# Kernel tuning notes

Hardware: AMD Instinct MI355X
Metric: run time of the kernel (lower is better)

The kernel has to match this reference:

```python
import jax, jax.numpy as jnp
import numpy as np

N, E, B = 50000, 400000, 16
H, D = 4, 64  # heads, per-head out feats
NUM_LAYERS = 4
NEG_SLOPE = 0.2


def setup_inputs() -> dict:
    key = jax.random.key(0)
    ks = jax.random.split(key, 12)
    inp = {
        "feat": jax.random.normal(ks[0], (N, 16), jnp.float32),
        "is_root": jax.random.uniform(ks[1], (N,), jnp.float32),
        "src": jax.random.randint(ks[2], (E,), 0, N, jnp.int32),
        "dst": jax.random.randint(ks[3], (E,), 0, N, jnp.int32),
        "graph_id": jnp.sort(jax.random.randint(ks[4], (N,), 0, B, jnp.int32)),
        "W_in": jax.random.normal(ks[5], (16, 64), jnp.float32) / jnp.sqrt(16.0),
        "b_in": jnp.zeros((64,), jnp.float32),
        "W_src": jax.random.normal(ks[6], (128, 256), jnp.float32) / jnp.sqrt(128.0),
        "b_src": jnp.zeros((256,), jnp.float32),
        "W_dst": jax.random.normal(ks[7], (128, 256), jnp.float32) / jnp.sqrt(128.0),
        "b_dst": jnp.zeros((256,), jnp.float32),
        "attn": jax.random.normal(ks[8], (H, D), jnp.float32) / jnp.sqrt(float(D)),
        "W_out": jax.random.normal(ks[9], (64, 32), jnp.float32) / jnp.sqrt(64.0),
        "b_out": jnp.zeros((32,), jnp.float32),
    }
    return inp


def _gatv2_layer(x, W_src, b_src, W_dst, b_dst, attn, src, dst, n_nodes):
    # DGL GATv2Conv: e_ij = a . LeakyReLU(W_src x_j + W_dst x_i); softmax over in-edges of i.
    fs = (x @ W_src + b_src).reshape(n_nodes, H, D)
    fd = (x @ W_dst + b_dst).reshape(n_nodes, H, D)
    e = jax.nn.leaky_relu(fs[src] + fd[dst], NEG_SLOPE)          # [E,H,D]
    logits = jnp.einsum("ehd,hd->eh", e, attn)                    # [E,H]
    m = jax.ops.segment_max(logits, dst, num_segments=n_nodes)    # [N,H]
    ex = jnp.exp(logits - m[dst])
    denom = jax.ops.segment_sum(ex, dst, num_segments=n_nodes)    # [N,H]
    alpha = ex / denom[dst]                                       # [E,H]
    msg = fs[src] * alpha[:, :, None]                             # [E,H,D]
    rst = jax.ops.segment_sum(msg, dst, num_segments=n_nodes)     # [N,H,D]
    return jnp.tanh(rst)


def reference(feat, is_root, src, dst, graph_id,
              W_in, b_in, W_src, b_src, W_dst, b_dst, attn, W_out, b_out):
    n_nodes = feat.shape[0]
    h0 = feat @ W_in + b_in                                       # [N,64]
    h = h0
    for _ in range(NUM_LAYERS):
        x = jnp.concatenate([h, h0], axis=1)                      # [N,128]
        h = _gatv2_layer(x, W_src, b_src, W_dst, b_dst, attn, src, dst, n_nodes).sum(axis=1)  # [N,64]
    hg = jax.ops.segment_sum(h * is_root[:, None], graph_id, num_segments=B)  # [B,64]
    return hg @ W_out + b_out                                     # [B,32]
```

## Files before the change

### kernel.cpp

```cpp
#include <hip/hip_runtime.h>
#include <math.h>

#define N_NODES 50000
#define N_EDGES 400000
#define N_GRAPHS 16
#define HEADS 4
#define NEG_SLOPE 0.2f
#define MAX_DEG 64

typedef __attribute__((ext_vector_type(8))) short short8;
typedef __attribute__((ext_vector_type(4))) float floatx4;
typedef _Float16 half_t;
typedef _Float16 half2_t __attribute__((ext_vector_type(2)));
typedef _Float16 half4_t __attribute__((ext_vector_type(4)));

__device__ __forceinline__ unsigned short f2bf(float x) {
    union { float f; unsigned int u; } v; v.f = x;
    unsigned int r = v.u + 0x7fffu + ((v.u >> 16) & 1u);
    return (unsigned short)(r >> 16);
}
__device__ __forceinline__ float bf2f(unsigned short b) {
    union { unsigned int u; float f; } v; v.u = ((unsigned int)b) << 16;
    return v.f;
}
__device__ __forceinline__ half2_t u2h2(unsigned int u) {
    union { unsigned int i; half2_t h; } v; v.i = u;
    return v.h;
}
__device__ __forceinline__ float fast_tanh(float x) {
    float e = __expf(2.f * x);
    return 1.f - 2.f / (e + 1.f);
}
__device__ __forceinline__ half2_t lrelu2(half2_t e) {
    half2_t s = e * (half2_t){(half_t)NEG_SLOPE, (half_t)NEG_SLOPE};
    return __builtin_elementwise_max(e, s);
}
__device__ __forceinline__ float dot2acc(half2_t a, half2_t b, float c) {
#if __has_builtin(__builtin_amdgcn_fdot2)
    return __builtin_amdgcn_fdot2(a, b, c, false);
#else
    return c + (float)a[0] * (float)b[0] + (float)a[1] * (float)b[1];
#endif
}

__global__ __launch_bounds__(256) void k_h0_pack(const float* __restrict__ feat,
                                                 const float* __restrict__ W_in,
                                                 const float* __restrict__ b_in,
                                                 unsigned short* __restrict__ h0,
                                                 const float* __restrict__ Wsrc,
                                                 const float* __restrict__ Wdst,
                                                 unsigned short* __restrict__ Wpack,
                                                 int* __restrict__ cursor,
                                                 float* __restrict__ hg) {
    int bid = blockIdx.x;
    if (bid < 12500) {
        int idx = bid * 256 + threadIdx.x;
        int node = idx >> 6, d = idx & 63;
        float acc = b_in[d];
        #pragma unroll
        for (int k = 0; k < 16; k++) acc += feat[node * 16 + k] * W_in[k * 64 + d];
        h0[idx] = f2bf(acc);
    } else if (bid < 12756) {
        int pb = bid - 12500;
        int mat = pb >> 7;
        int idx = (pb & 127) * 256 + threadIdx.x;
        const float* W = mat ? Wdst : Wsrc;
        int j = idx & 7;
        int lane = (idx >> 3) & 63;
        int q = (idx >> 9) & 3;
        int t = (idx >> 11) & 15;
        int col = t * 16 + (lane & 15);
        int k = q * 32 + (lane >> 4) * 8 + j;
        Wpack[mat * 32768 + idx] = f2bf(W[k * 256 + col]);
    } else if (bid < 12952) {
        int idx = (bid - 12756) * 256 + threadIdx.x;
        if (idx < N_NODES) cursor[idx] = 0;
    } else {
        for (int i = threadIdx.x; i < N_GRAPHS * 64; i += 256) hg[i] = 0.f;
    }
}

__global__ __launch_bounds__(256) void k_fill(const int* __restrict__ src, const int* __restrict__ dst,
                                              int* __restrict__ cursor, int* __restrict__ csr_pad, int e) {
    int i = blockIdx.x * 256 + threadIdx.x;
    if (i >= e) return;
    int d = dst[i];
    int slot = atomicAdd(&cursor[d], 1);
    if (slot < MAX_DEG) csr_pad[d * MAX_DEG + slot] = src[i];
}

__global__ __launch_bounds__(256) void k_gemm(const unsigned short* __restrict__ h,
                                              const unsigned short* __restrict__ h0,
                                              const unsigned short* __restrict__ Wpack,
                                              const float* __restrict__ bsrc,
                                              const float* __restrict__ bdst,
                                              half_t* __restrict__ fs,
                                              half_t* __restrict__ fd, int n) {
    __shared__ half_t tile[32][264];
    int mat = blockIdx.y;
    const unsigned short* Wp = Wpack + mat * 32768;
    const float* bias = mat ? bdst : bsrc;
    half_t* out = mat ? fd : fs;
    int wave = threadIdx.x >> 6, lane = threadIdx.x & 63;
    int quad = lane >> 4, m16 = lane & 15;
    int fhalf = wave & 1;
    int ngrp = wave >> 1;
    int node0 = blockIdx.x * 32 + ngrp * 16;

    floatx4 acc[8];
    #pragma unroll
    for (int t = 0; t < 8; t++) acc[t] = (floatx4){0.f, 0.f, 0.f, 0.f};

    int r = node0 + m16;
    if (r > n - 1) r = n - 1;

    #pragma unroll
    for (int q = 0; q < 4; q++) {
        int kk = q * 32 + quad * 8;
        const unsigned short* base = (kk < 64) ? (h + (size_t)r * 64 + kk)
                                               : (h0 + (size_t)r * 64 + (kk - 64));
        short8 x = *(const short8*)base;
        #pragma unroll
        for (int t = 0; t < 8; t++) {
            int tt = fhalf * 8 + t;
            short8 w = *(const short8*)(Wp + ((size_t)(tt * 4 + q) * 64 + lane) * 8);
            acc[t] = __builtin_amdgcn_mfma_f32_16x16x32_bf16(w, x, acc[t], 0, 0, 0);
        }
    }
    int lrow = ngrp * 16 + m16;
    #pragma unroll
    for (int t = 0; t < 8; t++) {
        int fbase = (fhalf * 8 + t) * 16 + quad * 4;
        float4 bb = *(const float4*)(bias + fbase);
        half4_t ov = { (half_t)(acc[t][0] + bb.x), (half_t)(acc[t][1] + bb.y),
                       (half_t)(acc[t][2] + bb.z), (half_t)(acc[t][3] + bb.w) };
        *(half4_t*)&tile[lrow][fbase] = ov;
    }
    __syncthreads();
    int base = blockIdx.x * 32;
    for (int i = threadIdx.x; i < 1024; i += 256) {
        int row = i >> 5, seg = i & 31;
        int node = base + row;
        if (node < n) {
            uint4 v = *(const uint4*)&tile[row][seg * 8];
            *(uint4*)(out + (size_t)node * 256 + seg * 8) = v;
        }
    }
}

__global__ __launch_bounds__(256) void k_agg(const half_t* __restrict__ fs,
                                             const half_t* __restrict__ fd,
                                             const int* __restrict__ cnt,
                                             const int* __restrict__ csr_pad,
                                             const float* __restrict__ attn,
                                             unsigned short* __restrict__ hout, int n) {
    int wave = threadIdx.x >> 6;
    int lane = threadIdx.x & 63;
    int node = blockIdx.x * 4 + wave;
    if (node >= n) return;
    int slot = lane >> 5;
    int foff = ((lane >> 3) & 3) * 64 + (lane & 7) * 8;
    unsigned boff = (unsigned)foff * 2;
    const char* fsb = (const char*)fs;

    half2_t at2[4];
    {
        float4 a0 = *(const float4*)(attn + foff);
        float4 a1 = *(const float4*)(attn + foff + 4);
        at2[0] = (half2_t){(half_t)a0.x, (half_t)a0.y};
        at2[1] = (half2_t){(half_t)a0.z, (half_t)a0.w};
        at2[2] = (half2_t){(half_t)a1.x, (half_t)a1.y};
        at2[3] = (half2_t){(half_t)a1.z, (half_t)a1.w};
    }
    half2_t fd2[4];
    {
        uint4 u = *(const uint4*)(fd + (size_t)node * 256 + foff);
        fd2[0] = u2h2(u.x); fd2[1] = u2h2(u.y); fd2[2] = u2h2(u.z); fd2[3] = u2h2(u.w);
    }

    int deg = cnt[node];
    if (deg > MAX_DEG) deg = MAX_DEG;
    int eid = 0;
    if (lane < deg) eid = csr_pad[node * MAX_DEG + lane];

    float l = 0.f;
    half2_t zero2 = {(half_t)0.f, (half_t)0.f};
    half2_t acc2[4] = {zero2, zero2, zero2, zero2};

    for (int j = 0; j < deg; j += 8) {
        int last = deg - 1;
        int i0 = j + slot, i1 = j + 2 + slot, i2 = j + 4 + slot, i3 = j + 6 + slot;
        bool v0 = i0 < deg, v1 = i1 < deg, v2 = i2 < deg, v3 = i3 < deg;
        int s0 = __shfl(eid, v0 ? i0 : last, 64);
        int s1 = __shfl(eid, v1 ? i1 : last, 64);
        int s2 = __shfl(eid, v2 ? i2 : last, 64);
        int s3 = __shfl(eid, v3 ? i3 : last, 64);
        uint4 g0 = *(const uint4*)(fsb + (((unsigned)s0 << 9) + boff));
        uint4 g1 = *(const uint4*)(fsb + (((unsigned)s1 << 9) + boff));
        uint4 g2 = *(const uint4*)(fsb + (((unsigned)s2 << 9) + boff));
        uint4 g3 = *(const uint4*)(fsb + (((unsigned)s3 << 9) + boff));
        half2_t f0[4] = {u2h2(g0.x), u2h2(g0.y), u2h2(g0.z), u2h2(g0.w)};
        half2_t f1[4] = {u2h2(g1.x), u2h2(g1.y), u2h2(g1.z), u2h2(g1.w)};
        half2_t f2[4] = {u2h2(g2.x), u2h2(g2.y), u2h2(g2.z), u2h2(g2.w)};
        half2_t f3[4] = {u2h2(g3.x), u2h2(g3.y), u2h2(g3.z), u2h2(g3.w)};
        float p0 = 0.f, p1 = 0.f, p2 = 0.f, p3 = 0.f;
        #pragma unroll
        for (int k = 0; k < 4; k++) {
            p0 = dot2acc(at2[k], lrelu2(f0[k] + fd2[k]), p0);
            p1 = dot2acc(at2[k], lrelu2(f1[k] + fd2[k]), p1);
            p2 = dot2acc(at2[k], lrelu2(f2[k] + fd2[k]), p2);
            p3 = dot2acc(at2[k], lrelu2(f3[k] + fd2[k]), p3);
        }
        p0 += __shfl_xor(p0, 1, 64); p1 += __shfl_xor(p1, 1, 64);
        p2 += __shfl_xor(p2, 1, 64); p3 += __shfl_xor(p3, 1, 64);
        p0 += __shfl_xor(p0, 2, 64); p1 += __shfl_xor(p1, 2, 64);
        p2 += __shfl_xor(p2, 2, 64); p3 += __shfl_xor(p3, 2, 64);
        p0 += __shfl_xor(p0, 4, 64); p1 += __shfl_xor(p1, 4, 64);
        p2 += __shfl_xor(p2, 4, 64); p3 += __shfl_xor(p3, 4, 64);
        float w0 = v0 ? __expf(fminf(p0, 80.f)) : 0.f;
        float w1 = v1 ? __expf(fminf(p1, 80.f)) : 0.f;
        float w2 = v2 ? __expf(fminf(p2, 80.f)) : 0.f;
        float w3 = v3 ? __expf(fminf(p3, 80.f)) : 0.f;
        l += (w0 + w1) + (w2 + w3);
        half_t hw0 = (half_t)w0, hw1 = (half_t)w1, hw2 = (half_t)w2, hw3 = (half_t)w3;
        half2_t w02 = {hw0, hw0}, w12 = {hw1, hw1}, w22 = {hw2, hw2}, w32 = {hw3, hw3};
        #pragma unroll
        for (int k = 0; k < 4; k++) {
            acc2[k] += w02 * f0[k];
            acc2[k] += w12 * f1[k];
            acc2[k] += w22 * f2[k];
            acc2[k] += w32 * f3[k];
        }
    }
    l += __shfl_xor(l, 32, 64);
    #pragma unroll
    for (int k = 0; k < 4; k++) {
        float t = __builtin_bit_cast(float, acc2[k]);
        t = __shfl_xor(t, 32, 64);
        acc2[k] += __builtin_bit_cast(half2_t, t);
    }

    float inv = (l > 0.f) ? 1.f / l : 0.f;
    half2_t a0 = slot ? acc2[2] : acc2[0];
    half2_t a1 = slot ? acc2[3] : acc2[1];
    float o0 = fast_tanh((float)a0[0] * inv);
    float o1 = fast_tanh((float)a0[1] * inv);
    float o2 = fast_tanh((float)a1[0] * inv);
    float o3 = fast_tanh((float)a1[1] * inv);
    o0 += __shfl_xor(o0, 8, 64);  o0 += __shfl_xor(o0, 16, 64);
    o1 += __shfl_xor(o1, 8, 64);  o1 += __shfl_xor(o1, 16, 64);
    o2 += __shfl_xor(o2, 8, 64);  o2 += __shfl_xor(o2, 16, 64);
    o3 += __shfl_xor(o3, 8, 64);  o3 += __shfl_xor(o3, 16, 64);
    if ((lane & 31) < 8) {
        ushort4 ov = {f2bf(o0), f2bf(o1), f2bf(o2), f2bf(o3)};
        *(ushort4*)(hout + (size_t)node * 64 + (lane & 7) * 8 + slot * 4) = ov;
    }
}

__global__ __launch_bounds__(256) void k_readout(const unsigned short* __restrict__ h,
                                                 const float* __restrict__ is_root,
                                                 const int* __restrict__ gid, float* __restrict__ hg, int n) {
    int wave = threadIdx.x >> 6, lane = threadIdx.x & 63;
    int start = blockIdx.x * 128 + wave * 32;
    if (start >= n) return;
    int stop = min(start + 32, n);
    float acc = 0.f;
    int cur = gid[start];
    for (int i = start; i < stop; i++) {
        int g = gid[i];
        if (g != cur) {
            atomicAdd(&hg[cur * 64 + lane], acc);
            acc = 0.f;
            cur = g;
        }
        acc += bf2f(h[(size_t)i * 64 + lane]) * is_root[i];
    }
    atomicAdd(&hg[cur * 64 + lane], acc);
}

__global__ __launch_bounds__(512) void k_out(const float* __restrict__ hg, const float* __restrict__ W_out,
                                             const float* __restrict__ b_out, float* __restrict__ out) {
    int t = threadIdx.x;
    if (t >= N_GRAPHS * 32) return;
    int b = t >> 5, c = t & 31;
    float a = b_out[c];
    #pragma unroll
    for (int d = 0; d < 64; d++) a += hg[b * 64 + d] * W_out[d * 32 + c];
    out[t] = a;
}

extern "C" void kernel_launch(void* const* d_in, const int* in_sizes, int n_in,
                              void* d_out, int out_size, void* d_ws, size_t ws_size,
                              hipStream_t stream) {
    const float* feat    = (const float*)d_in[0];
    const float* is_root = (const float*)d_in[1];
    const int*   src     = (const int*)d_in[2];
    const int*   dst     = (const int*)d_in[3];
    const int*   gid     = (const int*)d_in[4];
    const float* W_in    = (const float*)d_in[5];
    const float* b_in    = (const float*)d_in[6];
    const float* W_src   = (const float*)d_in[7];
    const float* b_src   = (const float*)d_in[8];
    const float* W_dst   = (const float*)d_in[9];
    const float* b_dst   = (const float*)d_in[10];
    const float* attn    = (const float*)d_in[11];
    const float* W_out   = (const float*)d_in[12];
    const float* b_out   = (const float*)d_in[13];
    float* out = (float*)d_out;

    char* ws = (char*)d_ws;
    size_t off = 0;
    auto take = [&](size_t bytes) -> char* {
        char* p = ws + off;
        off = (off + bytes + 255) & ~(size_t)255;
        return p;
    };
    half_t* fs            = (half_t*)take((size_t)N_NODES * 256 * 2);
    half_t* fd            = (half_t*)take((size_t)N_NODES * 256 * 2);
    unsigned short* h0    = (unsigned short*)take((size_t)N_NODES * 64 * 2);
    unsigned short* hA    = (unsigned short*)take((size_t)N_NODES * 64 * 2);
    unsigned short* hB    = (unsigned short*)take((size_t)N_NODES * 64 * 2);
    unsigned short* Wpack = (unsigned short*)take((size_t)2 * 32768 * 2);
    float* hg             = (float*)take((size_t)N_GRAPHS * 64 * 4);
    int*   cursor         = (int*)take((size_t)N_NODES * 4);
    int*   csr_pad        = (int*)take((size_t)N_NODES * MAX_DEG * 4);

    const int n = N_NODES, e = N_EDGES;
    dim3 b256(256);

    k_h0_pack<<<dim3(12953), b256, 0, stream>>>(feat, W_in, b_in, h0, W_src, W_dst, Wpack, cursor, hg);

    k_fill<<<dim3((e + 255) / 256), b256, 0, stream>>>(src, dst, cursor, csr_pad, e);

    const unsigned short* hin = h0;
    unsigned short* houts[4] = { hA, hB, hA, hB };
    for (int layer = 0; layer < 4; layer++) {
        k_gemm<<<dim3((n + 31) / 32, 2), b256, 0, stream>>>(hin, h0, Wpack, b_src, b_dst, fs, fd, n);
        k_agg<<<dim3((n + 3) / 4), b256, 0, stream>>>(fs, fd, cursor, csr_pad, attn, houts[layer], n);
        hin = houts[layer];
    }

    k_readout<<<dim3((n + 127) / 128), b256, 0, stream>>>(hB, is_root, gid, hg, n);
    k_out<<<dim3(1), dim3(512), 0, stream>>>(hg, W_out, b_out, out);
}
```

Before: 384.0 us.

## Store source features in FP8 and fuse CSR fill into the setup kernel

The source-projected features fs are now written as FP8 (e4m3) instead of FP16, which halves the bytes gathered per edge in the aggregation kernel. They are decoded back to half precision with hardware conversion builtins, with a software fallback when those are missing. Separately, the CSR fill is merged into the h0/pack setup kernel and the cursor is zeroed by a memset, removing one kernel launch. The FP8 storage trades accuracy in the attention logits and messages for less gather bandwidth.

```diff
diff --git a/kernel.cpp b/kernel.cpp
--- a/kernel.cpp
+++ b/kernel.cpp
@@ -8,8 +8,13 @@
 #define NEG_SLOPE 0.2f
 #define MAX_DEG 64
 
+#define H0_BLKS 12500
+#define PACK_BLKS 256
+#define FILL_BLKS 1563
+
 typedef __attribute__((ext_vector_type(8))) short short8;
 typedef __attribute__((ext_vector_type(4))) float floatx4;
+typedef __attribute__((ext_vector_type(2))) float floatx2;
 typedef _Float16 half_t;
 typedef _Float16 half2_t __attribute__((ext_vector_type(2)));
 typedef _Float16 half4_t __attribute__((ext_vector_type(4)));
@@ -40,6 +45,68 @@
     return __builtin_amdgcn_fdot2(a, b, c, false);
 #else
     return c + (float)a[0] * (float)b[0] + (float)a[1] * (float)b[1];
+#endif
+}
+__device__ __forceinline__ half2_t pkrtz(float x, float y) {
+#if __has_builtin(__builtin_amdgcn_cvt_pkrtz)
+    auto r = __builtin_amdgcn_cvt_pkrtz(x, y);
+    return __builtin_bit_cast(half2_t, r);
+#else
+    return (half2_t){(half_t)x, (half_t)y};
+#endif
+}
+
+#if __has_builtin(__builtin_amdgcn_cvt_pk_fp8_f32) && __has_builtin(__builtin_amdgcn_cvt_pk_f32_fp8)
+#define HW_FP8 1
+#else
+#define HW_FP8 0
+__device__ __forceinline__ unsigned char f2fp8_1(float x) {
+    unsigned char s = (x < 0.f) ? 0x80 : 0;
+    float a = fabsf(x);
+    if (a >= 448.f) return s | 0x7E;
+    if (a < ldexpf(1.f, -10)) return s;
+    int e; float fr = frexpf(a, &e);
+    int E = e - 1 + 7;
+    if (E <= 0) {
+        int q = (int)(a * ldexpf(1.f, 9) + 0.5f);
+        if (q > 7) { q = 0; E = 1; return s | (unsigned char)(E << 3); }
+        return s | (unsigned char)q;
+    }
+    int q = (int)(fr * 16.f + 0.5f);
+    if (q == 16) { q = 8; E++; }
+    if (E >= 15 && q > 14) return s | 0x7E;
+    return s | (unsigned char)((E << 3) | (q - 8));
+}
+__device__ __forceinline__ float fp8d(unsigned char b) {
+    int s = b >> 7, e = (b >> 3) & 15, m = b & 7;
+    float mag = e ? ldexpf(1.f + m * 0.125f, e - 7) : ldexpf(m * 0.125f, -6);
+    return s ? -mag : mag;
+}
+#endif
+
+__device__ __forceinline__ int pack_fp8x4(float a, float b, float c, float d) {
+#if HW_FP8
+    int u = __builtin_amdgcn_cvt_pk_fp8_f32(a, b, 0, false);
+    u = __builtin_amdgcn_cvt_pk_fp8_f32(c, d, u, true);
+    return u;
+#else
+    return (int)f2fp8_1(a) | ((int)f2fp8_1(b) << 8) | ((int)f2fp8_1(c) << 16) | ((int)f2fp8_1(d) << 24);
+#endif
+}
+__device__ __forceinline__ void fp8x8_to_h2(uint2 g, half2_t* f) {
+#if HW_FP8
+    floatx2 l0 = __builtin_amdgcn_cvt_pk_f32_fp8((int)g.x, false);
+    floatx2 h0 = __builtin_amdgcn_cvt_pk_f32_fp8((int)g.x, true);
+    floatx2 l1 = __builtin_amdgcn_cvt_pk_f32_fp8((int)g.y, false);
+    floatx2 h1 = __builtin_amdgcn_cvt_pk_f32_fp8((int)g.y, true);
+    f[0] = pkrtz(l0[0], l0[1]);
+    f[1] = pkrtz(h0[0], h0[1]);
+    f[2] = pkrtz(l1[0], l1[1]);
+    f[3] = pkrtz(h1[0], h1[1]);
+#else
+    unsigned char* p = (unsigned char*)&g;
+    #pragma unroll
+    for (int k = 0; k < 4; k++) f[k] = (half2_t){(half_t)fp8d(p[2*k]), (half_t)fp8d(p[2*k+1])};
 #endif
 }
 
@@ -50,18 +117,21 @@
                                                  const float* __restrict__ Wsrc,
                                                  const float* __restrict__ Wdst,
                                                  unsigned short* __restrict__ Wpack,
+                                                 const int* __restrict__ src,
+                                                 const int* __restrict__ dst,
                                                  int* __restrict__ cursor,
+                                                 int* __restrict__ csr_pad,
                                                  float* __restrict__ hg) {
     int bid = blockIdx.x;
-    if (bid < 12500) {
+    if (bid < H0_BLKS) {
         int idx = bid * 256 + threadIdx.x;
         int node = idx >> 6, d = idx & 63;
         float acc = b_in[d];
         #pragma unroll
         for (int k = 0; k < 16; k++) acc += feat[node * 16 + k] * W_in[k * 64 + d];
         h0[idx] = f2bf(acc);
-    } else if (bid < 12756) {
-        int pb = bid - 12500;
+    } else if (bid < H0_BLKS + PACK_BLKS) {
+        int pb = bid - H0_BLKS;
         int mat = pb >> 7;
         int idx = (pb & 127) * 256 + threadIdx.x;
         const float* W = mat ? Wdst : Wsrc;
@@ -72,21 +142,16 @@
         int col = t * 16 + (lane & 15);
         int k = q * 32 + (lane >> 4) * 8 + j;
         Wpack[mat * 32768 + idx] = f2bf(W[k * 256 + col]);
-    } else if (bid < 12952) {
-        int idx = (bid - 12756) * 256 + threadIdx.x;
-        if (idx < N_NODES) cursor[idx] = 0;
+    } else if (bid < H0_BLKS + PACK_BLKS + FILL_BLKS) {
+        int i = (bid - H0_BLKS - PACK_BLKS) * 256 + threadIdx.x;
+        if (i < N_EDGES) {
+            int d = dst[i];
+            int slot = atomicAdd(&cursor[d], 1);
+            if (slot < MAX_DEG) csr_pad[d * MAX_DEG + slot] = src[i];
+        }
     } else {
         for (int i = threadIdx.x; i < N_GRAPHS * 64; i += 256) hg[i] = 0.f;
     }
-}
-
-__global__ __launch_bounds__(256) void k_fill(const int* __restrict__ src, const int* __restrict__ dst,
-                                              int* __restrict__ cursor, int* __restrict__ csr_pad, int e) {
-    int i = blockIdx.x * 256 + threadIdx.x;
-    if (i >= e) return;
-    int d = dst[i];
-    int slot = atomicAdd(&cursor[d], 1);
-    if (slot < MAX_DEG) csr_pad[d * MAX_DEG + slot] = src[i];
 }
 
 __global__ __launch_bounds__(256) void k_gemm(const unsigned short* __restrict__ h,
@@ -94,13 +159,12 @@
                                               const unsigned short* __restrict__ Wpack,
                                               const float* __restrict__ bsrc,
                                               const float* __restrict__ bdst,
-                                              half_t* __restrict__ fs,
+                                              unsigned char* __restrict__ fs,
                                               half_t* __restrict__ fd, int n) {
-    __shared__ half_t tile[32][264];
+    __shared__ __align__(16) unsigned char tileb[32][528];
     int mat = blockIdx.y;
     const unsigned short* Wp = Wpack + mat * 32768;
     const float* bias = mat ? bdst : bsrc;
-    half_t* out = mat ? fd : fs;
     int wave = threadIdx.x >> 6, lane = threadIdx.x & 63;
     int quad = lane >> 4, m16 = lane & 15;
     int fhalf = wave & 1;
@@ -128,27 +192,49 @@
         }
     }
     int lrow = ngrp * 16 + m16;
-    #pragma unroll
-    for (int t = 0; t < 8; t++) {
-        int fbase = (fhalf * 8 + t) * 16 + quad * 4;
-        float4 bb = *(const float4*)(bias + fbase);
-        half4_t ov = { (half_t)(acc[t][0] + bb.x), (half_t)(acc[t][1] + bb.y),
-                       (half_t)(acc[t][2] + bb.z), (half_t)(acc[t][3] + bb.w) };
-        *(half4_t*)&tile[lrow][fbase] = ov;
+    if (mat == 0) {
+        #pragma unroll
+        for (int t = 0; t < 8; t++) {
+            int fbase = (fhalf * 8 + t) * 16 + quad * 4;
+            float4 bb = *(const float4*)(bias + fbase);
+            int u = pack_fp8x4(acc[t][0] + bb.x, acc[t][1] + bb.y,
+                               acc[t][2] + bb.z, acc[t][3] + bb.w);
+            *(int*)&tileb[lrow][fbase] = u;
+        }
+    } else {
+        #pragma unroll
+        for (int t = 0; t < 8; t++) {
+            int fbase = (fhalf * 8 + t) * 16 + quad * 4;
+            float4 bb = *(const float4*)(bias + fbase);
+            half4_t ov = { (half_t)(acc[t][0] + bb.x), (half_t)(acc[t][1] + bb.y),
+                           (half_t)(acc[t][2] + bb.z), (half_t)(acc[t][3] + bb.w) };
+            *(half4_t*)&tileb[lrow][fbase * 2] = ov;
+        }
     }
     __syncthreads();
     int base = blockIdx.x * 32;
-    for (int i = threadIdx.x; i < 1024; i += 256) {
-        int row = i >> 5, seg = i & 31;
-        int node = base + row;
-        if (node < n) {
-            uint4 v = *(const uint4*)&tile[row][seg * 8];
-            *(uint4*)(out + (size_t)node * 256 + seg * 8) = v;
-        }
-    }
-}
-
-__global__ __launch_bounds__(256) void k_agg(const half_t* __restrict__ fs,
+    if (mat == 0) {
+        for (int i = threadIdx.x; i < 512; i += 256) {
+            int row = i >> 4, seg = i & 15;
+            int node = base + row;
+            if (node < n) {
+                uint4 v = *(const uint4*)&tileb[row][seg * 16];
+                *(uint4*)(fs + (size_t)node * 256 + seg * 16) = v;
+            }
+        }
+    } else {
+        for (int i = threadIdx.x; i < 1024; i += 256) {
+            int row = i >> 5, seg = i & 31;
+            int node = base + row;
+            if (node < n) {
+                uint4 v = *(const uint4*)&tileb[row][seg * 16];
+                *(uint4*)((unsigned char*)fd + (size_t)node * 512 + seg * 16) = v;
+            }
+        }
+    }
+}
+
+__global__ __launch_bounds__(256) void k_agg(const unsigned char* __restrict__ fs,
                                              const half_t* __restrict__ fd,
                                              const int* __restrict__ cnt,
                                              const int* __restrict__ csr_pad,
@@ -160,8 +246,7 @@
     if (node >= n) return;
     int slot = lane >> 5;
     int foff = ((lane >> 3) & 3) * 64 + (lane & 7) * 8;
-    unsigned boff = (unsigned)foff * 2;
-    const char* fsb = (const char*)fs;
+    unsigned boff = (unsigned)foff;
 
     half2_t at2[4];
     {
@@ -195,14 +280,15 @@
         int s1 = __shfl(eid, v1 ? i1 : last, 64);
         int s2 = __shfl(eid, v2 ? i2 : last, 64);
         int s3 = __shfl(eid, v3 ? i3 : last, 64);
-        uint4 g0 = *(const uint4*)(fsb + (((unsigned)s0 << 9) + boff));
-        uint4 g1 = *(const uint4*)(fsb + (((unsigned)s1 << 9) + boff));
-        uint4 g2 = *(const uint4*)(fsb + (((unsigned)s2 << 9) + boff));
-        uint4 g3 = *(const uint4*)(fsb + (((unsigned)s3 << 9) + boff));
-        half2_t f0[4] = {u2h2(g0.x), u2h2(g0.y), u2h2(g0.z), u2h2(g0.w)};
-        half2_t f1[4] = {u2h2(g1.x), u2h2(g1.y), u2h2(g1.z), u2h2(g1.w)};
-        half2_t f2[4] = {u2h2(g2.x), u2h2(g2.y), u2h2(g2.z), u2h2(g2.w)};
-        half2_t f3[4] = {u2h2(g3.x), u2h2(g3.y), u2h2(g3.z), u2h2(g3.w)};
+        uint2 g0 = *(const uint2*)(fs + (((unsigned)s0 << 8) + boff));
+        uint2 g1 = *(const uint2*)(fs + (((unsigned)s1 << 8) + boff));
+        uint2 g2 = *(const uint2*)(fs + (((unsigned)s2 << 8) + boff));
+        uint2 g3 = *(const uint2*)(fs + (((unsigned)s3 << 8) + boff));
+        half2_t f0[4], f1[4], f2[4], f3[4];
+        fp8x8_to_h2(g0, f0);
+        fp8x8_to_h2(g1, f1);
+        fp8x8_to_h2(g2, f2);
+        fp8x8_to_h2(g3, f3);
         float p0 = 0.f, p1 = 0.f, p2 = 0.f, p3 = 0.f;
         #pragma unroll
         for (int k = 0; k < 4; k++) {
@@ -315,7 +401,7 @@
         off = (off + bytes + 255) & ~(size_t)255;
         return p;
     };
-    half_t* fs            = (half_t*)take((size_t)N_NODES * 256 * 2);
+    unsigned char* fs     = (unsigned char*)take((size_t)N_NODES * 256);
     half_t* fd            = (half_t*)take((size_t)N_NODES * 256 * 2);
     unsigned short* h0    = (unsigned short*)take((size_t)N_NODES * 64 * 2);
     unsigned short* hA    = (unsigned short*)take((size_t)N_NODES * 64 * 2);
@@ -325,12 +411,12 @@
     int*   cursor         = (int*)take((size_t)N_NODES * 4);
     int*   csr_pad        = (int*)take((size_t)N_NODES * MAX_DEG * 4);
 
-    const int n = N_NODES, e = N_EDGES;
+    const int n = N_NODES;
     dim3 b256(256);
 
-    k_h0_pack<<<dim3(12953), b256, 0, stream>>>(feat, W_in, b_in, h0, W_src, W_dst, Wpack, cursor, hg);
-
-    k_fill<<<dim3((e + 255) / 256), b256, 0, stream>>>(src, dst, cursor, csr_pad, e);
+    hipMemsetAsync(cursor, 0, (size_t)N_NODES * 4, stream);
+    k_h0_pack<<<dim3(H0_BLKS + PACK_BLKS + FILL_BLKS + 1), b256, 0, stream>>>(
+        feat, W_in, b_in, h0, W_src, W_dst, Wpack, src, dst, cursor, csr_pad, hg);
 
     const unsigned short* hin = h0;
     unsigned short* houts[4] = { hA, hB, hA, hB };
```

Result: slower. 399.2 us (+4.0%).
